# Kernel tuning notes

Measured on AMD Instinct MI355X. Metric: run time of the kernel, lower is better.

The kernel has to match this reference:

```python
import jax, jax.numpy as jnp
import numpy as np

B, T, P = 4, 512, 3584          # batch, new tokens per seq, cached tokens per seq
D_MODEL, H, KH, DH = 2048, 16, 4, 128
N_REP = H // KH
MAX_SEQ = 4096
ROPE_BASE = 1e6
EPS = 1e-6


def _rmsnorm(t, w):
    # t: [..., DH]
    var = jnp.mean(t * t, axis=-1, keepdims=True)
    return t * jax.lax.rsqrt(var + EPS) * w


def _rope(t, positions):
    # t: [N, heads, DH], positions: [N] int
    half = DH // 2
    inv_freq = (1.0 / ROPE_BASE) ** (2.0 * jnp.arange(half, dtype=jnp.float32) / DH)
    theta = positions.astype(jnp.float32)[:, None] * inv_freq[None, :]   # [N, half]
    theta = jnp.concatenate([theta, theta], axis=-1)                      # [N, DH]
    sin = jnp.sin(theta)[:, None, :]
    cos = jnp.cos(theta)[:, None, :]
    x1, x2 = jnp.split(t, 2, axis=-1)
    rot = jnp.concatenate([-x2, x1], axis=-1)
    return cos * t + sin * rot


def setup_inputs() -> dict:
    key = jax.random.key(0)
    ks = jax.random.split(key, 9)
    N = B * T
    x = jax.random.normal(ks[0], (N, D_MODEL), dtype=jnp.float32)
    k_cache = jax.random.normal(ks[1], (B, KH, P, DH), dtype=jnp.float32)
    v_cache = jax.random.normal(ks[2], (B, KH, P, DH), dtype=jnp.float32)
    s = 1.0 / np.sqrt(D_MODEL)
    w_q = jax.random.normal(ks[3], (H * DH, D_MODEL), dtype=jnp.float32) * s
    w_k = jax.random.normal(ks[4], (KH * DH, D_MODEL), dtype=jnp.float32) * s
    w_v = jax.random.normal(ks[5], (KH * DH, D_MODEL), dtype=jnp.float32) * s
    w_o = jax.random.normal(ks[6], (D_MODEL, H * DH), dtype=jnp.float32) * s
    q_norm_w = jnp.ones((DH,), dtype=jnp.float32)
    k_norm_w = jnp.ones((DH,), dtype=jnp.float32)
    # each sequence's new tokens occupy absolute positions [P, P+T)
    positions = jnp.tile(P + jnp.arange(T, dtype=jnp.int32), B)  # [B*T]
    return {"x": x, "k_cache": k_cache, "v_cache": v_cache,
            "w_q": w_q, "w_k": w_k, "w_v": w_v, "w_o": w_o,
            "q_norm_w": q_norm_w, "k_norm_w": k_norm_w,
            "positions": positions}


def reference(x, k_cache, v_cache, w_q, w_k, w_v, w_o, q_norm_w, k_norm_w, positions):
    N = x.shape[0]
    # QKV projections (no bias)
    q = (x @ w_q.T).reshape(N, H, DH)
    k = (x @ w_k.T).reshape(N, KH, DH)
    v = (x @ w_v.T).reshape(N, KH, DH)
    # per-head RMSNorm then RoPE at absolute positions
    q = _rope(_rmsnorm(q, q_norm_w), positions)
    k = _rope(_rmsnorm(k, k_norm_w), positions)
    # assemble full KV: cached (pre-rotated) past + new tokens
    k_new = k.reshape(B, T, KH, DH).transpose(0, 2, 1, 3)   # [B,KH,T,DH]
    v_new = v.reshape(B, T, KH, DH).transpose(0, 2, 1, 3)
    k_full = jnp.concatenate([k_cache, k_new], axis=2)       # [B,KH,P+T,DH]
    v_full = jnp.concatenate([v_cache, v_new], axis=2)
    # GQA: repeat each kv head n_rep times
    k_rep = jnp.repeat(k_full, N_REP, axis=1)                # [B,H,S,DH]
    v_rep = jnp.repeat(v_full, N_REP, axis=1)
    q4 = q.reshape(B, T, H, DH).transpose(0, 2, 1, 3)        # [B,H,T,DH]
    scale = 1.0 / jnp.sqrt(jnp.float32(DH))
    scores = jnp.einsum('bhtd,bhsd->bhts', q4, k_rep) * scale  # [B,H,T,P+T]
    # right-bottom causal mask: q_pos = P + t, kv_pos = s
    q_pos = P + jnp.arange(T)
    kv_pos = jnp.arange(P + T)
    mask = q_pos[:, None] >= kv_pos[None, :]
    scores = jnp.where(mask[None, None], scores, -jnp.inf)
    attn = jax.nn.softmax(scores, axis=-1)
    out = jnp.einsum('bhts,bhsd->bhtd', attn, v_rep)          # [B,H,T,DH]
    out = out.transpose(0, 2, 1, 3).reshape(N, H * DH)
    return out @ w_o.T
```

## Files before the change

### kernel.cpp

```cpp
#include <hip/hip_runtime.h>
#include <hip/hip_bf16.h>
#include <stdint.h>

#define B_   4
#define T_   512
#define P_   3584
#define S_   4096
#define H_   16
#define KH_  4
#define DM_  2048
#define DH_  128
#define NTOK 2048
#define NCHUNK 3
#define NTC  43
#define NROWS 32768

typedef __attribute__((ext_vector_type(8)))  short          bf16x8;
typedef __attribute__((ext_vector_type(4)))  float          f32x4;
typedef __attribute__((ext_vector_type(16))) float          f32x16;
typedef __attribute__((ext_vector_type(4)))  float          f4v;
typedef __attribute__((ext_vector_type(4)))  unsigned short us4v;

__device__ __forceinline__ unsigned short f2bf(float x) {
    union { float f; unsigned u; } v; v.f = x;
    unsigned r = v.u + 0x7FFFu + ((v.u >> 16) & 1u);
    return (unsigned short)(r >> 16);
}
__device__ __forceinline__ float bf2f(unsigned short b) {
    union { unsigned u; float f; } v; v.u = ((unsigned)b) << 16; return v.f;
}
__device__ __forceinline__ unsigned pkbf(float a, float b) {
    __hip_bfloat162 h = __float22bfloat162_rn(float2{a, b});
    union { __hip_bfloat162 h; unsigned u; } cv; cv.h = h; return cv.u;
}

#define GLDS16(gp, lp) __builtin_amdgcn_global_load_lds( \
    (const __attribute__((address_space(1))) void*)(gp), \
    (__attribute__((address_space(3))) void*)(lp), 16, 0, 0)

__global__ __launch_bounds__(256) void convert_all(
    const float* __restrict__ x,  const float* __restrict__ wq,
    const float* __restrict__ wk, const float* __restrict__ wv,
    const float* __restrict__ wo, const float* __restrict__ kc,
    unsigned short* __restrict__ xb,   unsigned short* __restrict__ wqkvb,
    unsigned short* __restrict__ wob,  unsigned short* __restrict__ kfull)
{
    const long total = 5505024;
    for (long i = (long)blockIdx.x * 256 + threadIdx.x; i < total;
         i += (long)gridDim.x * 256) {
        const f4v* src; us4v* dst; long s4, d4;
        if (i < 1048576)      { src=(const f4v*)x;  dst=(us4v*)xb;              s4=i;         d4=s4; }
        else if (i < 2097152) { src=(const f4v*)wq; dst=(us4v*)wqkvb;           s4=i-1048576; d4=s4; }
        else if (i < 2359296) { src=(const f4v*)wk; dst=(us4v*)(wqkvb+4194304); s4=i-2097152; d4=s4; }
        else if (i < 2621440) { src=(const f4v*)wv; dst=(us4v*)(wqkvb+5242880); s4=i-2359296; d4=s4; }
        else if (i < 3670016) { src=(const f4v*)wo; dst=(us4v*)wob;             s4=i-2621440; d4=s4; }
        else                  { s4=i-3670016; long bk=s4/114688;
                                d4=bk*131072+(s4-bk*114688);
                                src=(const f4v*)kc; dst=(us4v*)kfull; }
        f4v v = src[s4];
        us4v o; o[0]=f2bf(v[0]); o[1]=f2bf(v[1]); o[2]=f2bf(v[2]); o[3]=f2bf(v[3]);
        dst[d4] = o;
    }
}

__global__ __launch_bounds__(256) void vcache_transpose(
    const float* __restrict__ vc, unsigned short* __restrict__ vT)
{
    __shared__ unsigned short tile[64][65];
    const int bk = blockIdx.z;
    const int st = blockIdx.x;
    const int dt = blockIdx.y;
    const float* src = vc + ((size_t)bk * P_ + st * 64) * DH_ + dt * 64;
    const int tq = threadIdx.x & 15;
    const int ts = threadIdx.x >> 4;
    #pragma unroll
    for (int i = 0; i < 4; ++i) {
        const int si = ts + i * 16;
        f4v v = *(const f4v*)(src + (size_t)si * DH_ + tq * 4);
        tile[si][tq*4+0] = f2bf(v[0]); tile[si][tq*4+1] = f2bf(v[1]);
        tile[si][tq*4+2] = f2bf(v[2]); tile[si][tq*4+3] = f2bf(v[3]);
    }
    __syncthreads();
    unsigned short* dst = vT + ((size_t)bk * DH_ + dt * 64) * S_ + st * 64;
    const int sq = threadIdx.x & 15;
    const int td = threadIdx.x >> 4;
    #pragma unroll
    for (int i = 0; i < 4; ++i) {
        const int di = td + i * 16;
        us4v o;
        o[0] = tile[sq*4+0][di]; o[1] = tile[sq*4+1][di];
        o[2] = tile[sq*4+2][di]; o[3] = tile[sq*4+3][di];
        *(us4v*)(dst + (size_t)di * S_ + sq * 4) = o;
    }
}

__global__ __launch_bounds__(256) void gemm_bt(
    const unsigned short* __restrict__ A, const unsigned short* __restrict__ Bw,
    void* __restrict__ C, int M, int N, int K, int obf16)
{
    __shared__ short As[2][128 * 32];
    __shared__ short Bs[2][128 * 32];
    const int tid = threadIdx.x, lane = tid & 63, w = tid >> 6;
    const int nbn = N >> 7;
    const int bm = blockIdx.x / nbn, bn = blockIdx.x % nbn;
    const int m0 = bm << 7, n0 = bn << 7;
    const int wm = w >> 1, wn = w & 1;

    f32x4 acc[4][4];
    #pragma unroll
    for (int i = 0; i < 4; ++i)
        #pragma unroll
        for (int j = 0; j < 4; ++j)
            #pragma unroll
            for (int r = 0; r < 4; ++r) acc[i][j][r] = 0.f;

    const int arow = lane >> 2;
    const int acol = (lane & 3) << 3;

    auto stage = [&](int buf, int k0) {
        #pragma unroll
        for (int cc = 0; cc < 2; ++cc) {
            const int c = 2 * w + cc;
            GLDS16(A  + (size_t)(m0 + c * 16 + arow) * K + k0 + acol, &As[buf][c * 512]);
            GLDS16(Bw + (size_t)(n0 + c * 16 + arow) * K + k0 + acol, &Bs[buf][c * 512]);
        }
    };

    stage(0, 0);
    __syncthreads();

    const int nk = K >> 5;
    const int fr = lane & 15, fk = (lane >> 4) << 3;
    for (int t = 0; t < nk; ++t) {
        const int buf = t & 1;
        if (t + 1 < nk) stage(buf ^ 1, (t + 1) << 5);
        bf16x8 a[4], b[4];
        #pragma unroll
        for (int i = 0; i < 4; ++i)
            a[i] = *(const bf16x8*)&As[buf][(wm * 64 + i * 16 + fr) * 32 + fk];
        #pragma unroll
        for (int j = 0; j < 4; ++j)
            b[j] = *(const bf16x8*)&Bs[buf][(wn * 64 + j * 16 + fr) * 32 + fk];
        #pragma unroll
        for (int i = 0; i < 4; ++i)
            #pragma unroll
            for (int j = 0; j < 4; ++j)
                acc[i][j] = __builtin_amdgcn_mfma_f32_16x16x32_bf16(a[i], b[j], acc[i][j], 0, 0, 0);
        __syncthreads();
    }

    const int er = lane >> 4, ec = lane & 15;
    #pragma unroll
    for (int i = 0; i < 4; ++i)
        #pragma unroll
        for (int j = 0; j < 4; ++j)
            #pragma unroll
            for (int r = 0; r < 4; ++r) {
                const int row = m0 + wm * 64 + i * 16 + er * 4 + r;
                const int col = n0 + wn * 64 + j * 16 + ec;
                if (obf16) ((unsigned short*)C)[(size_t)row * N + col] = f2bf(acc[i][j][r]);
                else       ((float*)C)[(size_t)row * N + col] = acc[i][j][r];
            }
}

__global__ __launch_bounds__(64) void norm_rope(
    const unsigned short* __restrict__ qkv, const float* __restrict__ qw,
    const float* __restrict__ kw,  const int* __restrict__ pos,
    unsigned short* __restrict__ Qb, unsigned short* __restrict__ Kf,
    unsigned short* __restrict__ VT)
{
    const int task = blockIdx.x;
    const int n = task / 24, idx = task % 24;
    const int lane = threadIdx.x;
    const int b = n >> 9, t = n & 511;

    if (idx >= 20) {
        const int kh = idx - 20;
        const unsigned short* src = qkv + (size_t)n * 3072 + 2560 + kh * 128;
        unsigned short* dstT = VT + (size_t)(b * KH_ + kh) * DH_ * S_ + (P_ + t);
        dstT[(size_t)lane * S_]        = src[lane];
        dstT[(size_t)(lane + 64) * S_] = src[lane + 64];
        return;
    }
    const bool isq = idx < 16;
    const int hh = isq ? idx : (idx - 16);
    const unsigned short* src = qkv + (size_t)n * 3072 + (isq ? hh * 128 : 2048 + hh * 128);
    const float* wn_ = isq ? qw : kw;
    float x0 = bf2f(src[lane]), x1 = bf2f(src[lane + 64]);
    float ss = x0 * x0 + x1 * x1;
    #pragma unroll
    for (int m = 1; m < 64; m <<= 1) ss += __shfl_xor(ss, m);
    const float rinv = rsqrtf(ss * (1.0f / 128.0f) + 1e-6f);
    float y0 = x0 * rinv * wn_[lane];
    float y1 = x1 * rinv * wn_[lane + 64];
    const float fr = __expf(-(float)lane * (13.815510557964274f / 64.0f));
    const float th = (float)pos[n] * fr;
    float sn, cs; sincosf(th, &sn, &cs);
    float o0 = cs * y0 - sn * y1;
    float o1 = cs * y1 + sn * y0;
    unsigned short* dst;
    if (isq) {
        o0 *= 0.08838834764831845f; o1 *= 0.08838834764831845f;
        dst = Qb + ((size_t)(b * H_ + hh) * T_ + t) * DH_;
    } else {
        dst = Kf + ((size_t)(b * KH_ + hh) * S_ + P_ + t) * DH_;
    }
    dst[lane]      = f2bf(o0);
    dst[lane + 64] = f2bf(o1);
}

__global__ __launch_bounds__(256, 3) void attn(
    const unsigned short* __restrict__ Qb, const unsigned short* __restrict__ Kf,
    const unsigned short* __restrict__ VT, unsigned short* __restrict__ op0,
    unsigned short* __restrict__ op1, unsigned short* __restrict__ op2,
    float2* __restrict__ ml)
{
    __shared__ short Ks[2][32 * 128];
    __shared__ short Vs[2][128 * 32];

    const int tid = threadIdx.x, lane = tid & 63, w = tid >> 6;
    const int c = blockIdx.x >> 8;
    const int rest = blockIdx.x & 255;
    const int qt = rest & 3;
    const int bh = rest >> 2;
    const int h = bh & 15, b = bh >> 4;
    const int kvh = h >> 2;
    const int t0 = qt * 128;

    const unsigned short* Qrow = Qb + (size_t)(b * H_ + h) * T_ * DH_;
    const unsigned short* Kb   = Kf + (size_t)(b * KH_ + kvh) * S_ * DH_;
    const unsigned short* VTb  = VT + (size_t)(b * KH_ + kvh) * DH_ * S_;

    const int ql = lane & 31;
    const int hi = lane >> 5;

    bf16x8 qf[8];
    {
        const unsigned short* qp = Qrow + (size_t)(t0 + w * 32 + ql) * DH_ + hi * 8;
        #pragma unroll
        for (int d0 = 0; d0 < 8; ++d0) qf[d0] = *(const bf16x8*)(qp + d0 * 16);
    }

    f32x16 o[4];
    #pragma unroll
    for (int d = 0; d < 4; ++d)
        #pragma unroll
        for (int r = 0; r < 16; ++r) o[d][r] = 0.f;
    float m_run = -INFINITY, l_run = 0.f;

    const int q_pos = P_ + t0 + w * 32 + ql;
    const int s_end_wave = P_ + t0 + w * 32 + 32;
    const int nt_full = (P_ + t0 + 128) >> 5;
    const int tstart = c * NTC;
    const int tend = min(tstart + NTC, nt_full);

    auto stage = [&](int buf, int tile) {
        const int s0 = tile << 5;
        #pragma unroll
        for (int cc = 0; cc < 2; ++cc) {
            const int cx = 2 * w + cc;
            const int krow = cx * 4 + (lane >> 4);
            const int kel  = 8 * ((lane & 15) ^ (krow & 15));
            GLDS16(Kb + (size_t)(s0 + krow) * DH_ + kel, &Ks[buf][cx * 512]);
            const int vrow = cx * 16 + (lane >> 2);
            const int vel  = 8 * ((lane & 3) ^ ((lane >> 3) & 3));
            GLDS16(VTb + (size_t)vrow * S_ + s0 + vel, &Vs[buf][cx * 512]);
        }
    };

    stage(0, tstart);
    __syncthreads();

    for (int i = 0, t = tstart; t < tend; ++t, ++i) {
        const int buf = i & 1;
        const int s0 = t << 5;
        if (t + 1 < tend) stage(buf ^ 1, t + 1);
        if (s0 < s_end_wave) {
            f32x16 st;
            #pragma unroll
            for (int r = 0; r < 16; ++r) st[r] = 0.f;
            {
                const char* kbase = (const char*)&Ks[buf][0] + ql * 256;
                const int sw = 16 * (ql & 15);
                #pragma unroll
                for (int d0 = 0; d0 < 8; ++d0) {
                    bf16x8 kfr = *(const bf16x8*)(kbase + ((d0 * 32 + 16 * hi) ^ sw));
                    st = __builtin_amdgcn_mfma_f32_32x32x16_bf16(kfr, qf[d0], st, 0, 0, 0);
                }
            }
            if (s0 + 31 > P_ + t0 + w * 32) {
                #pragma unroll
                for (int r = 0; r < 16; ++r) {
                    const int srow = (r & 3) + 8 * (r >> 2) + 4 * hi;
                    if (s0 + srow > q_pos) st[r] = -INFINITY;
                }
            }
            float pmax = st[0];
            #pragma unroll
            for (int r = 1; r < 16; ++r) pmax = fmaxf(pmax, st[r]);
            pmax = fmaxf(pmax, __shfl_xor(pmax, 32));
            if (!__all(pmax <= m_run + 8.f)) {
                const float m_new = fmaxf(m_run, pmax);
                const float alpha = __expf(m_run - m_new);
                l_run *= alpha;
                #pragma unroll
                for (int r = 0; r < 16; ++r) {
                    const int qr = (r & 3) + 8 * (r >> 2) + 4 * hi;
                    const float a = __shfl(alpha, qr);
                    #pragma unroll
                    for (int d = 0; d < 4; ++d) o[d][r] *= a;
                }
                m_run = m_new;
            }
            float p[16]; float psum = 0.f;
            #pragma unroll
            for (int r = 0; r < 16; ++r) { p[r] = __expf(st[r] - m_run); psum += p[r]; }
            psum += __shfl_xor(psum, 32);
            l_run += psum;
            unsigned pk[8];
            #pragma unroll
            for (int u = 0; u < 8; ++u) pk[u] = pkbf(p[2 * u], p[2 * u + 1]);
            unsigned xw[8];
            #pragma unroll
            for (int u = 0; u < 8; ++u) xw[u] = (unsigned)__shfl_xor((int)pk[u], 32);
            union { bf16x8 v; unsigned u[4]; } pa0, pa1;
            pa0.u[0] = hi ? xw[2] : pk[0];  pa0.u[1] = hi ? xw[3] : pk[1];
            pa0.u[2] = hi ? pk[2] : xw[0];  pa0.u[3] = hi ? pk[3] : xw[1];
            pa1.u[0] = hi ? xw[6] : pk[4];  pa1.u[1] = hi ? xw[7] : pk[5];
            pa1.u[2] = hi ? pk[6] : xw[4];  pa1.u[3] = hi ? pk[7] : xw[5];
            #pragma unroll
            for (int ch = 0; ch < 2; ++ch)
                #pragma unroll
                for (int db = 0; db < 4; ++db) {
                    const int vrow = db * 32 + ql;
                    bf16x8 vf = *(const bf16x8*)&Vs[buf][vrow * 32 + 8 * ((2 * ch + hi) ^ ((ql >> 1) & 3))];
                    o[db] = __builtin_amdgcn_mfma_f32_32x32x16_bf16(
                        ch ? pa1.v : pa0.v, vf, o[db], 0, 0, 0);
                }
        }
        __syncthreads();
    }

    unsigned short* op = (c == 0) ? op0 : (c == 1) ? op1 : op2;
    const int rowbase = (b * H_ + h) * T_ + t0 + w * 32;
    if (hi == 0) ml[c * NROWS + rowbase + ql] = float2{m_run, l_run};
    #pragma unroll
    for (int r = 0; r < 16; ++r) {
        const int qr = (r & 3) + 8 * (r >> 2) + 4 * hi;
        unsigned short* orow = op + (size_t)(rowbase + qr) * DH_;
        #pragma unroll
        for (int d = 0; d < 4; ++d)
            orow[d * 32 + ql] = f2bf(o[d][r]);
    }
}

__global__ __launch_bounds__(256) void combine(
    const float2* __restrict__ ml,
    const unsigned short* __restrict__ op0, const unsigned short* __restrict__ op1,
    const unsigned short* __restrict__ op2, unsigned short* __restrict__ ao)
{
    const int row = blockIdx.x * 4 + (threadIdx.x >> 6);
    const int lane = threadIdx.x & 63;
    const float2 a0 = ml[row], a1 = ml[NROWS + row], a2 = ml[2 * NROWS + row];
    const float m = fmaxf(a0.x, fmaxf(a1.x, a2.x));
    const float w0 = __expf(a0.x - m), w1 = __expf(a1.x - m), w2 = __expf(a2.x - m);
    const float Linv = 1.0f / (w0 * a0.y + w1 * a1.y + w2 * a2.y);
    const size_t src = (size_t)row * DH_ + 2 * lane;
    const unsigned u0 = *(const unsigned*)(op0 + src);
    const unsigned u1 = *(const unsigned*)(op1 + src);
    const unsigned u2 = *(const unsigned*)(op2 + src);
    const float v0 = (bf2f((unsigned short)u0) * w0 + bf2f((unsigned short)u1) * w1 +
                      bf2f((unsigned short)u2) * w2) * Linv;
    const float v1 = (bf2f((unsigned short)(u0 >> 16)) * w0 + bf2f((unsigned short)(u1 >> 16)) * w1 +
                      bf2f((unsigned short)(u2 >> 16)) * w2) * Linv;
    const int t = row & 511, h = (row >> 9) & 15, b = row >> 13;
    unsigned short* dst = ao + ((size_t)(b * T_ + t) * (H_ * DH_)) + h * DH_ + 2 * lane;
    *(unsigned*)dst = pkbf(v0, v1);
}

extern "C" void kernel_launch(void* const* d_in, const int* in_sizes, int n_in,
                              void* d_out, int out_size, void* d_ws, size_t ws_size,
                              hipStream_t stream)
{
    const float* x   = (const float*)d_in[0];
    const float* kc  = (const float*)d_in[1];
    const float* vc  = (const float*)d_in[2];
    const float* wq  = (const float*)d_in[3];
    const float* wk  = (const float*)d_in[4];
    const float* wv  = (const float*)d_in[5];
    const float* wo  = (const float*)d_in[6];
    const float* qnw = (const float*)d_in[7];
    const float* knw = (const float*)d_in[8];
    const int*   pos = (const int*)d_in[9];
    float* out = (float*)d_out;

    char* ws = (char*)d_ws;
    unsigned short* xb    = (unsigned short*)(ws + 0);
    unsigned short* wqkvb = (unsigned short*)(ws + 8388608);
    unsigned short* wob   = (unsigned short*)(ws + 20971520);
    unsigned short* qkvb  = (unsigned short*)(ws + 29360128);
    unsigned short* qb    = (unsigned short*)(ws + 41943040);
    unsigned short* kfull = (unsigned short*)(ws + 50331648);
    unsigned short* vT    = (unsigned short*)(ws + 67108864);
    unsigned short* ao    = (unsigned short*)(ws + 83886080);
    unsigned short* op0   = (unsigned short*)(ws + 0);
    unsigned short* op1   = (unsigned short*)(ws + 8388608);
    float2*         ml    = (float2*)(ws + 16777216);
    unsigned short* op2   = (unsigned short*)(ws + 29360128);

    hipLaunchKernelGGL(convert_all, dim3(2048), dim3(256), 0, stream,
                       x, wq, wk, wv, wo, kc, xb, wqkvb, wob, kfull);
    hipLaunchKernelGGL(vcache_transpose, dim3(P_ / 64, 2, B_ * KH_), dim3(256), 0, stream,
                       vc, vT);
    hipLaunchKernelGGL(gemm_bt, dim3(16 * 24), dim3(256), 0, stream,
                       xb, wqkvb, (void*)qkvb, 2048, 3072, 2048, 1);
    hipLaunchKernelGGL(norm_rope, dim3(NTOK * 24), dim3(64), 0, stream,
                       qkvb, qnw, knw, pos, qb, kfull, vT);
    hipLaunchKernelGGL(attn, dim3(NCHUNK * 256), dim3(256), 0, stream,
                       qb, kfull, vT, op0, op1, op2, ml);
    hipLaunchKernelGGL(combine, dim3(NROWS / 4), dim3(256), 0, stream,
                       ml, op0, op1, op2, ao);
    hipLaunchKernelGGL(gemm_bt, dim3(16 * 16), dim3(256), 0, stream,
                       ao, wob, (void*)out, 2048, 2048, 2048, 0);
}
```

Before: 233.8 us.

## Split attention KV into four chunks and use base-2 exp with folded log2e

Raises the split-KV chunk count from 3 to 4, so there are more attention blocks (1024) and each block walks fewer KV tiles. Occupancy hint goes to 4 blocks per SM, and the combine kernel now merges four partials. The log2e factor is folded into the Q scale so the softmax can use the raw v_exp_f32 instruction, and max3 reduces the row-max cost. It also loosens the rescale threshold to match the base-2 domain. The trade-offs are an extra workspace buffer, more combine traffic, and register pressure that may rise under the higher occupancy bound.

After: 331.7 us. 1.42x slower.

```diff
diff --git a/kernel.cpp b/kernel.cpp
--- a/kernel.cpp
+++ b/kernel.cpp
@@ -11,8 +11,8 @@
 #define DM_  2048
 #define DH_  128
 #define NTOK 2048
-#define NCHUNK 3
-#define NTC  43
+#define NCHUNK 4
+#define NTC  32
 #define NROWS 32768
 
 typedef __attribute__((ext_vector_type(8)))  short          bf16x8;
@@ -32,6 +32,12 @@
 __device__ __forceinline__ unsigned pkbf(float a, float b) {
     __hip_bfloat162 h = __float22bfloat162_rn(float2{a, b});
     union { __hip_bfloat162 h; unsigned u; } cv; cv.h = h; return cv.u;
+}
+__device__ __forceinline__ float ex2(float x) {
+    float r; asm("v_exp_f32 %0, %1" : "=v"(r) : "v"(x)); return r;
+}
+__device__ __forceinline__ float max3f(float a, float b, float c) {
+    float r; asm("v_max3_f32 %0, %1, %2, %3" : "=v"(r) : "v"(a), "v"(b), "v"(c)); return r;
 }
 
 #define GLDS16(gp, lp) __builtin_amdgcn_global_load_lds( \
@@ -200,7 +206,8 @@
     float o1 = cs * y1 + sn * y0;
     unsigned short* dst;
     if (isq) {
-        o0 *= 0.08838834764831845f; o1 *= 0.08838834764831845f;
+        const float qs = 0.08838834764831845f * 1.4426950408889634f;
+        o0 *= qs; o1 *= qs;
         dst = Qb + ((size_t)(b * H_ + hh) * T_ + t) * DH_;
     } else {
         dst = Kf + ((size_t)(b * KH_ + hh) * S_ + P_ + t) * DH_;
@@ -209,11 +216,11 @@
     dst[lane + 64] = f2bf(o1);
 }
 
-__global__ __launch_bounds__(256, 3) void attn(
+__global__ __launch_bounds__(256, 4) void attn(
     const unsigned short* __restrict__ Qb, const unsigned short* __restrict__ Kf,
     const unsigned short* __restrict__ VT, unsigned short* __restrict__ op0,
     unsigned short* __restrict__ op1, unsigned short* __restrict__ op2,
-    float2* __restrict__ ml)
+    unsigned short* __restrict__ op3, float2* __restrict__ ml)
 {
     __shared__ short Ks[2][32 * 128];
     __shared__ short Vs[2][128 * 32];
@@ -295,13 +302,14 @@
                     if (s0 + srow > q_pos) st[r] = -INFINITY;
                 }
             }
-            float pmax = st[0];
-            #pragma unroll
-            for (int r = 1; r < 16; ++r) pmax = fmaxf(pmax, st[r]);
+            float m0_ = max3f(st[0], st[1], st[2]),  m1_ = max3f(st[3], st[4], st[5]);
+            float m2_ = max3f(st[6], st[7], st[8]),  m3_ = max3f(st[9], st[10], st[11]);
+            float m4_ = max3f(st[12], st[13], st[14]);
+            float pmax = fmaxf(max3f(m0_, m1_, m2_), max3f(m3_, m4_, st[15]));
             pmax = fmaxf(pmax, __shfl_xor(pmax, 32));
-            if (!__all(pmax <= m_run + 8.f)) {
+            if (!__all(pmax <= m_run + 11.5f)) {
                 const float m_new = fmaxf(m_run, pmax);
-                const float alpha = __expf(m_run - m_new);
+                const float alpha = ex2(m_run - m_new);
                 l_run *= alpha;
                 #pragma unroll
                 for (int r = 0; r < 16; ++r) {
@@ -314,7 +322,7 @@
             }
             float p[16]; float psum = 0.f;
             #pragma unroll
-            for (int r = 0; r < 16; ++r) { p[r] = __expf(st[r] - m_run); psum += p[r]; }
+            for (int r = 0; r < 16; ++r) { p[r] = ex2(st[r] - m_run); psum += p[r]; }
             psum += __shfl_xor(psum, 32);
             l_run += psum;
             unsigned pk[8];
@@ -341,7 +349,7 @@
         __syncthreads();
     }
 
-    unsigned short* op = (c == 0) ? op0 : (c == 1) ? op1 : op2;
+    unsigned short* op = (c == 0) ? op0 : (c == 1) ? op1 : (c == 2) ? op2 : op3;
     const int rowbase = (b * H_ + h) * T_ + t0 + w * 32;
     if (hi == 0) ml[c * NROWS + rowbase + ql] = float2{m_run, l_run};
     #pragma unroll
@@ -357,22 +365,26 @@
 __global__ __launch_bounds__(256) void combine(
     const float2* __restrict__ ml,
     const unsigned short* __restrict__ op0, const unsigned short* __restrict__ op1,
-    const unsigned short* __restrict__ op2, unsigned short* __restrict__ ao)
+    const unsigned short* __restrict__ op2, const unsigned short* __restrict__ op3,
+    unsigned short* __restrict__ ao)
 {
     const int row = blockIdx.x * 4 + (threadIdx.x >> 6);
     const int lane = threadIdx.x & 63;
-    const float2 a0 = ml[row], a1 = ml[NROWS + row], a2 = ml[2 * NROWS + row];
-    const float m = fmaxf(a0.x, fmaxf(a1.x, a2.x));
-    const float w0 = __expf(a0.x - m), w1 = __expf(a1.x - m), w2 = __expf(a2.x - m);
-    const float Linv = 1.0f / (w0 * a0.y + w1 * a1.y + w2 * a2.y);
+    const float2 a0 = ml[row], a1 = ml[NROWS + row];
+    const float2 a2 = ml[2 * NROWS + row], a3 = ml[3 * NROWS + row];
+    const float m = fmaxf(fmaxf(a0.x, a1.x), fmaxf(a2.x, a3.x));
+    const float w0 = ex2(a0.x - m), w1 = ex2(a1.x - m);
+    const float w2 = ex2(a2.x - m), w3 = ex2(a3.x - m);
+    const float Linv = 1.0f / (w0 * a0.y + w1 * a1.y + w2 * a2.y + w3 * a3.y);
     const size_t src = (size_t)row * DH_ + 2 * lane;
     const unsigned u0 = *(const unsigned*)(op0 + src);
     const unsigned u1 = *(const unsigned*)(op1 + src);
     const unsigned u2 = *(const unsigned*)(op2 + src);
+    const unsigned u3 = *(const unsigned*)(op3 + src);
     const float v0 = (bf2f((unsigned short)u0) * w0 + bf2f((unsigned short)u1) * w1 +
-                      bf2f((unsigned short)u2) * w2) * Linv;
+                      bf2f((unsigned short)u2) * w2 + bf2f((unsigned short)u3) * w3) * Linv;
     const float v1 = (bf2f((unsigned short)(u0 >> 16)) * w0 + bf2f((unsigned short)(u1 >> 16)) * w1 +
-                      bf2f((unsigned short)(u2 >> 16)) * w2) * Linv;
+                      bf2f((unsigned short)(u2 >> 16)) * w2 + bf2f((unsigned short)(u3 >> 16)) * w3) * Linv;
     const int t = row & 511, h = (row >> 9) & 15, b = row >> 13;
     unsigned short* dst = ao + ((size_t)(b * T_ + t) * (H_ * DH_)) + h * DH_ + 2 * lane;
     *(unsigned*)dst = pkbf(v0, v1);
@@ -407,6 +419,7 @@
     unsigned short* op1   = (unsigned short*)(ws + 8388608);
     float2*         ml    = (float2*)(ws + 16777216);
     unsigned short* op2   = (unsigned short*)(ws + 29360128);
+    unsigned short* op3   = (unsigned short*)(ws + 92274688);
 
     hipLaunchKernelGGL(convert_all, dim3(2048), dim3(256), 0, stream,
                        x, wq, wk, wv, wo, kc, xb, wqkvb, wob, kfull);
@@ -417,9 +430,9 @@
     hipLaunchKernelGGL(norm_rope, dim3(NTOK * 24), dim3(64), 0, stream,
                        qkvb, qnw, knw, pos, qb, kfull, vT);
     hipLaunchKernelGGL(attn, dim3(NCHUNK * 256), dim3(256), 0, stream,
-                       qb, kfull, vT, op0, op1, op2, ml);
+                       qb, kfull, vT, op0, op1, op2, op3, ml);
     hipLaunchKernelGGL(combine, dim3(NROWS / 4), dim3(256), 0, stream,
-                       ml, op0, op1, op2, ao);
+                       ml, op0, op1, op2, op3, ao);
     hipLaunchKernelGGL(gemm_bt, dim3(16 * 16), dim3(256), 0, stream,
                        ao, wob, (void*)out, 2048, 2048, 2048, 0);
 }
```
